# Performance work log

Measured on AMD Instinct MI355X. Metric: run time of the kernel, lower is better.

The kernel has to match this reference:

```python
import jax, jax.numpy as jnp
import numpy as np

D_MODEL = 1024
N_HEADS = 16
D_HEAD = D_MODEL // N_HEADS
MAX_K_LEN = 1024
SYNTH_HIDDEN = 1024
B, TQ, TK = 2, 1024, 1024
CAUSAL = True


def setup_inputs() -> dict:
    key = jax.random.key(0)
    ks = jax.random.split(key, 12)
    s = 1.0 / np.sqrt(D_MODEL)
    inp = {
        "x_q": jax.random.normal(ks[0], (B, TQ, D_MODEL), jnp.float32),
        "x_kv": jax.random.normal(ks[1], (B, TK, D_MODEL), jnp.float32),
        "key_padding_mask": jnp.ones((B, TK), jnp.int32),
        # projection weights stored [in, out] (equivalent to torch Linear)
        "Wq": jax.random.normal(ks[2], (D_MODEL, D_MODEL), jnp.float32) * s,
        "bq": jnp.zeros((D_MODEL,), jnp.float32),
        "Wk": jax.random.normal(ks[3], (D_MODEL, D_MODEL), jnp.float32) * s,
        "bk": jnp.zeros((D_MODEL,), jnp.float32),
        "Wv": jax.random.normal(ks[4], (D_MODEL, D_MODEL), jnp.float32) * s,
        "bv": jnp.zeros((D_MODEL,), jnp.float32),
        "Wo": jax.random.normal(ks[5], (D_MODEL, D_MODEL), jnp.float32) * s,
        "bo": jnp.zeros((D_MODEL,), jnp.float32),
        # synthesizer MLP: d_model -> synth_hidden -> n_heads*max_k_len
        "Ws1": jax.random.normal(ks[6], (D_MODEL, SYNTH_HIDDEN), jnp.float32) * s,
        "bs1": jnp.zeros((SYNTH_HIDDEN,), jnp.float32),
        "Ws2": jax.random.normal(ks[7], (SYNTH_HIDDEN, N_HEADS * MAX_K_LEN), jnp.float32) * (1.0 / np.sqrt(SYNTH_HIDDEN)),
        "bs2": jnp.zeros((N_HEADS * MAX_K_LEN,), jnp.float32),
        # gate logits init at log(0.5/0.5) = 0 -> sigmoid = 0.5
        "gate": jnp.zeros((N_HEADS,), jnp.float32),
    }
    return inp


def _attention(x_q, x_kv, key_padding_mask, Wq, bq, Wk, bk, Wv, bv, Wo, bo,
               Ws1, bs1, Ws2, bs2, gate):
    B_, Tq, _ = x_q.shape
    Tk = x_kv.shape[1]
    scale = D_HEAD ** -0.5

    def shape_heads(x):  # [B,T,D] -> [B,H,T,dh]
        return x.reshape(B_, -1, N_HEADS, D_HEAD).transpose(0, 2, 1, 3)

    Q = shape_heads(x_q @ Wq + bq)
    K = shape_heads(x_kv @ Wk + bk)
    V = shape_heads(x_kv @ Wv + bv)

    vanilla = jnp.einsum("bhqd,bhkd->bhqk", Q, K) * scale

    # dense synthesizer: MLP(x_q) -> [B,Tq,H,max_k_len] -> [B,H,Tq,Tk]
    h = jax.nn.gelu(x_q @ Ws1 + bs1, approximate=False)
    S = (h @ Ws2 + bs2).reshape(B_, Tq, N_HEADS, MAX_K_LEN)
    synth = S.transpose(0, 2, 1, 3)[:, :, :, :Tk]

    g = jax.nn.sigmoid(gate).reshape(1, N_HEADS, 1, 1)
    logits = (1.0 - g) * vanilla + g * synth

    # key padding mask: 1 = keep, 0 = pad
    keep = (key_padding_mask > 0).reshape(B_, 1, 1, Tk)
    logits = jnp.where(keep, logits, -jnp.inf)
    if CAUSAL:
        causal_mask = jnp.tril(jnp.ones((Tq, Tk), bool))  # keep lower triangle
        logits = jnp.where(causal_mask, logits, -jnp.inf)

    attn = jax.nn.softmax(logits, axis=-1)
    ctx = jnp.einsum("bhqk,bhkd->bhqd", attn, V)
    out = ctx.transpose(0, 2, 1, 3).reshape(B_, Tq, D_MODEL)
    return out @ Wo + bo


def reference(x_q, x_kv, key_padding_mask, Wq, bq, Wk, bk, Wv, bv, Wo, bo,
              Ws1, bs1, Ws2, bs2, gate):
    return _attention(x_q, x_kv, key_padding_mask, Wq, bq, Wk, bk, Wv, bv,
                      Wo, bo, Ws1, bs1, Ws2, bs2, gate)
```

## Files before the change

kernel.cpp:

```cpp
#include <hip/hip_runtime.h>
#include <hip/hip_bf16.h>

#define D_MODEL 1024
#define N_HEADS 16
#define MAX_K_LEN 1024
#define B_SZ 2
#define TQ 1024
#define TK 1024
#define M_ROWS 2048
#define NKL 16384

using bf16x8 = __attribute__((ext_vector_type(8))) short;
using f32x4  = __attribute__((ext_vector_type(4))) float;
using u16x8  = __attribute__((ext_vector_type(8))) unsigned short;

__device__ __forceinline__ unsigned short f2b(float f) {
    unsigned u = __float_as_uint(f);
    u = (u + 0x7FFFu + ((u >> 16) & 1u)) >> 16;
    return (unsigned short)u;
}
__device__ __forceinline__ float b2f(unsigned short u) {
    return __uint_as_float(((unsigned)u) << 16);
}

__device__ __forceinline__ void async_cp16(void* lds, const void* g) {
    __builtin_amdgcn_global_load_lds(
        (__attribute__((address_space(1))) void*)(void*)g,
        (__attribute__((address_space(3))) void*)lds, 16, 0, 0);
}

__device__ __forceinline__ int xrow(int row) {
    return (row & 7) ^ (((row >> 3) & 3) << 1);
}

__device__ __forceinline__ void ptile128_core(
    const unsigned short* __restrict__ A, const unsigned short* __restrict__ Wt,
    const float* __restrict__ bias, unsigned short* __restrict__ C,
    int N, int m0g, int n0g, int act, const float* __restrict__ gate,
    unsigned short* lds)
{
    constexpr int NT = 32;
    const int tid = threadIdx.x;
    const int lane = tid & 63;
    const int fr = lane & 15, rg = lane >> 4;
    const int w = tid >> 6;
    const int wr = w >> 1, wc = w & 1;

    const int sr = tid >> 2;
    const int sc = ((tid & 3) ^ ((sr >> 1) & 3)) * 8;
    const unsigned short* gA = A  + (size_t)(m0g + sr) * 1024 + sc;
    const unsigned short* gB = Wt + (size_t)(n0g + sr) * 1024 + sc;

    auto stage = [&](int t) {
        unsigned short* bufA = lds + (t % 3) * 8192;
        unsigned short* bufB = bufA + 4096;
        const int k0 = t * 32;
        async_cp16(bufA + tid*8,        gA + k0);
        async_cp16(bufA + 2048 + tid*8, gA + (size_t)64*1024 + k0);
        async_cp16(bufB + tid*8,        gB + k0);
        async_cp16(bufB + 2048 + tid*8, gB + (size_t)64*1024 + k0);
    };

    f32x4 acc[4][4];
#pragma unroll
    for (int i = 0; i < 4; ++i)
#pragma unroll
        for (int j = 0; j < 4; ++j) { f32x4 z = {0.f,0.f,0.f,0.f}; acc[i][j] = z; }

    const int fko = (rg ^ ((fr >> 1) & 3)) * 8;

    stage(0); stage(1);
    asm volatile("s_waitcnt vmcnt(4)" ::: "memory");
    __builtin_amdgcn_s_barrier();
    __builtin_amdgcn_sched_barrier(0);

    for (int t = 0; t < NT; ++t) {
        const unsigned short* bufA = lds + (t % 3) * 8192;
        const unsigned short* bufB = bufA + 4096;

        bf16x8 afr[4], bfr[4];
#pragma unroll
        for (int mi = 0; mi < 4; ++mi)
            afr[mi] = *(const bf16x8*)(bufA + (wr*64 + mi*16 + fr)*32 + fko);
#pragma unroll
        for (int ni = 0; ni < 4; ++ni)
            bfr[ni] = *(const bf16x8*)(bufB + (wc*64 + ni*16 + fr)*32 + fko);
        if (t + 2 < NT) stage(t + 2);

        __builtin_amdgcn_s_setprio(1);
#pragma unroll
        for (int mi = 0; mi < 4; ++mi)
#pragma unroll
            for (int ni = 0; ni < 4; ++ni)
                acc[mi][ni] = __builtin_amdgcn_mfma_f32_16x16x32_bf16(
                    afr[mi], bfr[ni], acc[mi][ni], 0, 0, 0);
        __builtin_amdgcn_s_setprio(0);

        if (t < NT - 2)       asm volatile("s_waitcnt vmcnt(4)" ::: "memory");
        else if (t == NT - 2) asm volatile("s_waitcnt vmcnt(0)" ::: "memory");
        __builtin_amdgcn_s_barrier();
        __builtin_amdgcn_sched_barrier(0);
    }

    float qs = 1.f;
    if (act == 2) {
        const float gg = 1.f / (1.f + __expf(-gate[(n0g + wc*64) >> 6]));
        qs = (1.f - gg) * 0.125f;
    }

    unsigned short* scr = lds + w * 1024;
    float bv[4];
#pragma unroll
    for (int ni = 0; ni < 4; ++ni) bv[ni] = bias[n0g + wc*64 + ni*16 + fr];
    const int ro = lane >> 3;
    const int co = (lane & 7) * 8;
#pragma unroll
    for (int mi = 0; mi < 4; ++mi) {
#pragma unroll
        for (int ni = 0; ni < 4; ++ni)
#pragma unroll
            for (int r = 0; r < 4; ++r) {
                float c = acc[mi][ni][r] + bv[ni];
                if (act == 1) c = 0.5f * c * (1.f + erff(c * 0.70710678118654752f));
                else if (act == 2) c *= qs;
                scr[(rg*4 + r)*64 + ni*16 + fr] = f2b(c);
            }
#pragma unroll
        for (int p = 0; p < 2; ++p) {
            const int row = p*8 + ro;
            const u16x8 v = *(const u16x8*)(scr + row*64 + co);
            *(u16x8*)(C + (size_t)(m0g + wr*64 + mi*16 + row) * N + n0g + wc*64 + co) = v;
        }
    }
}

struct QkvhArgs {
    const unsigned short* A[4];
    const unsigned short* W[4];
    const float* bias[4];
    void* out[4];
    const float* gate;
};

__global__ __launch_bounds__(256, 3) void gemm_qkvh_p(QkvhArgs args) {
    __shared__ __align__(16) unsigned short lds[24576];
    const int z = blockIdx.z;
    const int m0 = (blockIdx.x >> 3) * 128;
    const int n0 = (blockIdx.x & 7) * 128;
    const int act = (z == 3) ? 1 : ((z == 0) ? 2 : 0);
    ptile128_core(args.A[z], args.W[z], args.bias[z],
                  (unsigned short*)args.out[z], D_MODEL, m0, n0, act, args.gate, lds);
}

__global__ __launch_bounds__(256, 3) void gemm_logits_p(
    const unsigned short* __restrict__ A, const unsigned short* __restrict__ Wt,
    const float* __restrict__ bias, unsigned short* __restrict__ C,
    const unsigned short* __restrict__ Qpre, const unsigned short* __restrict__ Kb)
{
    __shared__ __align__(16) unsigned short lds[24576];
    constexpr int NT = 34;
    const int bid = blockIdx.x;
    const int xcd = bid & 7;
    const int i = bid >> 3;
    const int hi = (i >= 72) ? 1 : 0;
    const int head = xcd * 2 + hi;
    const int j = i - hi * 72;
    int kq, idx;
    if (j < 16)      { kq = 0; idx = j; }
    else if (j < 30) { kq = 1; idx = j - 16; }
    else if (j < 42) { kq = 2; idx = j - 30; }
    else if (j < 52) { kq = 3; idx = j - 42; }
    else if (j < 60) { kq = 4; idx = j - 52; }
    else if (j < 66) { kq = 5; idx = j - 60; }
    else if (j < 70) { kq = 6; idx = j - 66; }
    else             { kq = 7; idx = j - 70; }
    const int b = idx & 1;
    const int rq = kq + (idx >> 1);
    const int m0g = (b * 8 + rq) * 128;
    const int n0g = (head * 8 + kq) * 128;

    const int tid = threadIdx.x;
    const int lane = tid & 63;
    const int fr = lane & 15, rg = lane >> 4;
    const int w = tid >> 6;
    const int wr = w >> 1, wc = w & 1;

    const int sr = tid >> 2;
    const int sc = ((tid & 3) ^ ((sr >> 1) & 3)) * 8;
    const unsigned short* gA = A  + (size_t)(m0g + sr) * 1024 + sc;
    const unsigned short* gB = Wt + (size_t)(n0g + sr) * 1024 + sc;
    const int q0 = rq * 128, k0a = kq * 128;
    const unsigned short* gA2 = Qpre + (size_t)(b*TQ + q0 + sr) * 1024 + head*64 + sc;
    const unsigned short* gB2 = Kb   + (size_t)(b*TK + k0a + sr) * 1024 + head*64 + sc;

    auto stageQK = [&](int t) {
        unsigned short* bufA = lds + (t % 3) * 8192;
        unsigned short* bufB = bufA + 4096;
        const int k0 = t * 32;
        async_cp16(bufA + tid*8,        gA2 + k0);
        async_cp16(bufA + 2048 + tid*8, gA2 + (size_t)64*1024 + k0);
        async_cp16(bufB + tid*8,        gB2 + k0);
        async_cp16(bufB + 2048 + tid*8, gB2 + (size_t)64*1024 + k0);
    };
    auto stageS = [&](int t) {
        unsigned short* bufA = lds + (t % 3) * 8192;
        unsigned short* bufB = bufA + 4096;
        const int k0 = (t - 2) * 32;
        async_cp16(bufA + tid*8,        gA + k0);
        async_cp16(bufA + 2048 + tid*8, gA + (size_t)64*1024 + k0);
        async_cp16(bufB + tid*8,        gB + k0);
        async_cp16(bufB + 2048 + tid*8, gB + (size_t)64*1024 + k0);
    };

    f32x4 acc[4][4];
#pragma unroll
    for (int ii = 0; ii < 4; ++ii)
#pragma unroll
        for (int jj = 0; jj < 4; ++jj) { f32x4 z = {0.f,0.f,0.f,0.f}; acc[ii][jj] = z; }

    const int fko = (rg ^ ((fr >> 1) & 3)) * 8;

    stageQK(0); stageQK(1);
    asm volatile("s_waitcnt vmcnt(4)" ::: "memory");
    __builtin_amdgcn_s_barrier();
    __builtin_amdgcn_sched_barrier(0);

    for (int t = 0; t < NT; ++t) {
        const unsigned short* bufA = lds + (t % 3) * 8192;
        const unsigned short* bufB = bufA + 4096;

        bf16x8 afr[4], bfr[4];
#pragma unroll
        for (int mi = 0; mi < 4; ++mi)
            afr[mi] = *(const bf16x8*)(bufA + (wr*64 + mi*16 + fr)*32 + fko);
#pragma unroll
        for (int ni = 0; ni < 4; ++ni)
            bfr[ni] = *(const bf16x8*)(bufB + (wc*64 + ni*16 + fr)*32 + fko);
        if (t + 2 < NT) stageS(t + 2);

        __builtin_amdgcn_s_setprio(1);
#pragma unroll
        for (int mi = 0; mi < 4; ++mi)
#pragma unroll
            for (int ni = 0; ni < 4; ++ni)
                acc[mi][ni] = __builtin_amdgcn_mfma_f32_16x16x32_bf16(
                    afr[mi], bfr[ni], acc[mi][ni], 0, 0, 0);
        __builtin_amdgcn_s_setprio(0);

        if (t < NT - 2)       asm volatile("s_waitcnt vmcnt(4)" ::: "memory");
        else if (t == NT - 2) asm volatile("s_waitcnt vmcnt(0)" ::: "memory");
        __builtin_amdgcn_s_barrier();
        __builtin_amdgcn_sched_barrier(0);
    }

    unsigned short* scr = lds + w * 1024;
    float bv[4];
#pragma unroll
    for (int ni = 0; ni < 4; ++ni) bv[ni] = bias[n0g + wc*64 + ni*16 + fr];
    const int ro = lane >> 3;
    const int co = (lane & 7) * 8;
#pragma unroll
    for (int mi = 0; mi < 4; ++mi) {
#pragma unroll
        for (int ni = 0; ni < 4; ++ni)
#pragma unroll
            for (int r = 0; r < 4; ++r)
                scr[(rg*4 + r)*64 + ni*16 + fr] = f2b(acc[mi][ni][r] + bv[ni]);
#pragma unroll
        for (int p = 0; p < 2; ++p) {
            const int row = p*8 + ro;
            const u16x8 v = *(const u16x8*)(scr + row*64 + co);
            *(u16x8*)(C + (size_t)(m0g + wr*64 + mi*16 + row) * NKL + n0g + wc*64 + co) = v;
        }
    }
}

__global__ __launch_bounds__(256, 3) void gemm_out_p(
    const unsigned short* __restrict__ A, const unsigned short* __restrict__ Wt,
    const float* __restrict__ bias, float* __restrict__ C)
{
    __shared__ __align__(16) unsigned short lds[24576];
    constexpr int NT = 32;
    const int m0g = blockIdx.y * 128;
    const int n0g = blockIdx.x * 128;

    const int tid = threadIdx.x;
    const int lane = tid & 63;
    const int fr = lane & 15, rg = lane >> 4;
    const int w = tid >> 6;
    const int wr = w >> 1, wc = w & 1;

    const int sr = tid >> 2;
    const int sc = ((tid & 3) ^ ((sr >> 1) & 3)) * 8;
    const unsigned short* gA = A  + (size_t)(m0g + sr) * 1024 + sc;
    const unsigned short* gB = Wt + (size_t)(n0g + sr) * 1024 + sc;

    auto stage = [&](int t) {
        unsigned short* bufA = lds + (t % 3) * 8192;
        unsigned short* bufB = bufA + 4096;
        const int k0 = t * 32;
        async_cp16(bufA + tid*8,        gA + k0);
        async_cp16(bufA + 2048 + tid*8, gA + (size_t)64*1024 + k0);
        async_cp16(bufB + tid*8,        gB + k0);
        async_cp16(bufB + 2048 + tid*8, gB + (size_t)64*1024 + k0);
    };

    f32x4 acc[4][4];
#pragma unroll
    for (int i = 0; i < 4; ++i)
#pragma unroll
        for (int j = 0; j < 4; ++j) { f32x4 z = {0.f,0.f,0.f,0.f}; acc[i][j] = z; }

    const int fko = (rg ^ ((fr >> 1) & 3)) * 8;

    stage(0); stage(1);
    asm volatile("s_waitcnt vmcnt(4)" ::: "memory");
    __builtin_amdgcn_s_barrier();
    __builtin_amdgcn_sched_barrier(0);

    for (int t = 0; t < NT; ++t) {
        const unsigned short* bufA = lds + (t % 3) * 8192;
        const unsigned short* bufB = bufA + 4096;

        bf16x8 afr[4], bfr[4];
#pragma unroll
        for (int mi = 0; mi < 4; ++mi)
            afr[mi] = *(const bf16x8*)(bufA + (wr*64 + mi*16 + fr)*32 + fko);
#pragma unroll
        for (int ni = 0; ni < 4; ++ni)
            bfr[ni] = *(const bf16x8*)(bufB + (wc*64 + ni*16 + fr)*32 + fko);
        if (t + 2 < NT) stage(t + 2);

        __builtin_amdgcn_s_setprio(1);
#pragma unroll
        for (int mi = 0; mi < 4; ++mi)
#pragma unroll
            for (int ni = 0; ni < 4; ++ni)
                acc[mi][ni] = __builtin_amdgcn_mfma_f32_16x16x32_bf16(
                    afr[mi], bfr[ni], acc[mi][ni], 0, 0, 0);
        __builtin_amdgcn_s_setprio(0);

        if (t < NT - 2)       asm volatile("s_waitcnt vmcnt(4)" ::: "memory");
        else if (t == NT - 2) asm volatile("s_waitcnt vmcnt(0)" ::: "memory");
        __builtin_amdgcn_s_barrier();
        __builtin_amdgcn_sched_barrier(0);
    }

#pragma unroll
    for (int ni = 0; ni < 4; ++ni) {
        const int colx = n0g + wc*64 + ni*16 + fr;
        const float bvv = bias[colx];
#pragma unroll
        for (int mi = 0; mi < 4; ++mi)
#pragma unroll
            for (int r = 0; r < 4; ++r) {
                const int row = m0g + wr*64 + mi*16 + rg*4 + r;
                C[(size_t)row * D_MODEL + colx] = acc[mi][ni][r] + bvv;
            }
    }
}

struct PrepArgs {
    const float* xq; const float* xkv;
    unsigned short* xq_b; unsigned short* xkv_b;
    const float* W[6]; unsigned short* Wt[6]; int Nw[6];
    const float* bs2; float* bs2g; const float* gate;
};

__global__ __launch_bounds__(256) void prep_all(PrepArgs p) {
    __shared__ float T[32][33];
    int id = blockIdx.x;
    if (id < 4096) {
        const float* src = (id < 2048) ? p.xq : p.xkv;
        unsigned short* dst = (id < 2048) ? p.xq_b : p.xkv_b;
        const int i = (id & 2047) * 256 + threadIdx.x;
        const float4 v = ((const float4*)src)[i];
        ushort4 o; o.x = f2b(v.x); o.y = f2b(v.y); o.z = f2b(v.z); o.w = f2b(v.w);
        ((ushort4*)dst)[i] = o;
        return;
    }
    if (id >= 25600) {
        const int i = (id - 25600) * 256 + threadIdx.x;
        const float gg = 1.f / (1.f + __expf(-p.gate[i >> 10]));
        p.bs2g[i] = gg * p.bs2[i];
        return;
    }
    id -= 4096;
    int seg, lb;
    if (id < 5120) { seg = id >> 10; lb = id & 1023; }
    else           { seg = 5;        lb = id - 5120; }
    const int N = p.Nw[seg];
    const int nx = N >> 5;
    const int bx = lb % nx, by = lb / nx;
    const int n0 = bx * 32, k0 = by * 32;
    const float* W = p.W[seg];
    unsigned short* Wt = p.Wt[seg];
    float gs = 1.f;
    if (seg == 5) gs = 1.f / (1.f + __expf(-p.gate[n0 >> 10]));
    const int r = threadIdx.x >> 3, c = (threadIdx.x & 7) * 4;
    const float4 v = *(const float4*)&W[(size_t)(k0 + r) * N + n0 + c];
    T[r][c] = v.x; T[r][c+1] = v.y; T[r][c+2] = v.z; T[r][c+3] = v.w;
    __syncthreads();
    ushort4 o;
    o.x = f2b(T[c][r] * gs); o.y = f2b(T[c+1][r] * gs);
    o.z = f2b(T[c+2][r] * gs); o.w = f2b(T[c+3][r] * gs);
    *(ushort4*)&Wt[(size_t)(n0 + r) * D_MODEL + k0 + c] = o;
}

__global__ __launch_bounds__(256) void attn_l(
    const unsigned short* __restrict__ Lb, const unsigned short* __restrict__ Vb,
    const int* __restrict__ kpm, unsigned short* __restrict__ ctx)
{
    const int bx = blockIdx.x;
    const int q1 = bx >> 1;
    const int qt = (bx & 1) ? q1 : (15 - q1);
    const int h = blockIdx.y, b = blockIdx.z;
    const int tid = threadIdx.x;
    const int lane = tid & 63;
    const int w = tid >> 6;
    const int col = lane & 15, rg = lane >> 4;
    const int q0g = qt * 64;

    __shared__ __align__(16) unsigned short Ls[2][64*64];
    __shared__ __align__(16) unsigned short Vt[2][64*64];
    __shared__ __align__(16) unsigned short Pl[4*16*64];

    const int srr = tid >> 3, scp = tid & 7;
    auto issueL = [&](int kt, int buf) {
        const unsigned short* gs = Lb + ((size_t)(b*TQ + q0g)) * NKL + h*MAX_K_LEN + kt*64;
        async_cp16(Ls[buf] + tid*8,        gs + (size_t)srr*NKL + (scp ^ xrow(srr))*8);
        async_cp16(Ls[buf] + 2048 + tid*8, gs + (size_t)(srr+32)*NKL + (scp ^ xrow(srr+32))*8);
    };
    const int vk = tid >> 2, vdc = (tid & 3) * 16;
    const int vkc = vk >> 3, vke = vk & 7;
    u16x8 vr0, vr1;
    auto loadV = [&](int kt) {
        const unsigned short* gv = Vb + ((size_t)(b*TK + kt*64 + vk)) * D_MODEL + h*64 + vdc;
        vr0 = *(const u16x8*)gv;
        vr1 = *(const u16x8*)(gv + 8);
    };
    auto writeV = [&](int buf) {
#pragma unroll
        for (int j = 0; j < 8; ++j) {
            const int d0 = vdc + j, d1 = vdc + 8 + j;
            Vt[buf][d0*64 + (vkc ^ xrow(d0))*8 + vke] = vr0[j];
            Vt[buf][d1*64 + (vkc ^ xrow(d1))*8 + vke] = vr1[j];
        }
    };

    issueL(0, 0);
    loadV(0);
    writeV(0);
    __syncthreads();

    unsigned short* Pw = Pl + w*(16*64);

    float mrun[4] = {-INFINITY,-INFINITY,-INFINITY,-INFINITY};
    float lrun[4] = {0.f,0.f,0.f,0.f};
    f32x4 octx[4];
#pragma unroll
    for (int n = 0; n < 4; ++n) { f32x4 z = {0.f,0.f,0.f,0.f}; octx[n] = z; }

    for (int kt = 0; kt <= qt; ++kt) {
        const int cur = kt & 1;

        int kvalid[4];
#pragma unroll
        for (int n = 0; n < 4; ++n)
            kvalid[n] = kpm[b*TK + kt*64 + n*16 + col];
        if (kt < qt) { issueL(kt + 1, cur ^ 1); loadV(kt + 1); }

        const bool diag = (kt == qt);
        float acc[4][4];
        float tmax[4] = {-INFINITY,-INFINITY,-INFINITY,-INFINITY};
#pragma unroll
        for (int n = 0; n < 4; ++n) {
            const int kl = n*16 + col;
#pragma unroll
            for (int r = 0; r < 4; ++r) {
                const int ql = w*16 + rg*4 + r;
                const float lv = b2f(Ls[cur][ql*64 + (((kl>>3) ^ xrow(ql)))*8 + (kl&7)]);
                const bool ok = (kvalid[n] > 0) && (!diag || kl <= ql);
                const float sv = ok ? lv : -INFINITY;
                acc[n][r] = sv;
                tmax[r] = fmaxf(tmax[r], sv);
            }
        }
#pragma unroll
        for (int o = 1; o < 16; o <<= 1) {
#pragma unroll
            for (int r = 0; r < 4; ++r) tmax[r] = fmaxf(tmax[r], __shfl_xor(tmax[r], o));
        }
        float sc[4];
#pragma unroll
        for (int r = 0; r < 4; ++r) {
            const float mn = fmaxf(mrun[r], tmax[r]);
            sc[r] = (mrun[r] == -INFINITY) ? 0.f : __expf(mrun[r] - mn);
            mrun[r] = mn;
        }
        float tsum[4] = {0.f,0.f,0.f,0.f};
#pragma unroll
        for (int n = 0; n < 4; ++n)
#pragma unroll
            for (int r = 0; r < 4; ++r) {
                const float pz = (acc[n][r] == -INFINITY) ? 0.f : __expf(acc[n][r] - mrun[r]);
                acc[n][r] = pz;
                tsum[r] += pz;
            }
#pragma unroll
        for (int o = 1; o < 16; o <<= 1) {
#pragma unroll
            for (int r = 0; r < 4; ++r) tsum[r] += __shfl_xor(tsum[r], o);
        }
#pragma unroll
        for (int r = 0; r < 4; ++r) lrun[r] = lrun[r]*sc[r] + tsum[r];
#pragma unroll
        for (int n = 0; n < 4; ++n)
#pragma unroll
            for (int r = 0; r < 4; ++r) octx[n][r] *= sc[r];

#pragma unroll
        for (int n = 0; n < 4; ++n) {
            const int kc = n*16 + col;
#pragma unroll
            for (int r = 0; r < 4; ++r) {
                const int q = rg*4 + r;
                Pw[q*64 + (((kc>>3) ^ xrow(q)))*8 + (kc&7)] = f2b(acc[n][r]);
            }
        }

#pragma unroll
        for (int ks = 0; ks < 2; ++ks) {
            const bf16x8 pa = *(const bf16x8*)(Pw + col*64 + ((ks*4 + rg) ^ xrow(col))*8);
#pragma unroll
            for (int n = 0; n < 4; ++n) {
                const int d = n*16 + col;
                const bf16x8 vv = *(const bf16x8*)(Vt[cur] + d*64 + ((ks*4 + rg) ^ xrow(d))*8);
                octx[n] = __builtin_amdgcn_mfma_f32_16x16x32_bf16(pa, vv, octx[n], 0, 0, 0);
            }
        }

        if (kt < qt) writeV(cur ^ 1);
        __syncthreads();
    }

    float inv[4];
#pragma unroll
    for (int r = 0; r < 4; ++r) inv[r] = (lrun[r] > 0.f) ? 1.f/lrun[r] : 0.f;
#pragma unroll
    for (int n = 0; n < 4; ++n)
#pragma unroll
        for (int r = 0; r < 4; ++r) {
            const size_t row = (size_t)(b*TQ + q0g + w*16 + rg*4 + r);
            ctx[row*D_MODEL + h*64 + n*16 + col] = f2b(octx[n][r]*inv[r]);
        }
}

extern "C" void kernel_launch(void* const* d_in, const int* in_sizes, int n_in,
                              void* d_out, int out_size, void* d_ws, size_t ws_size,
                              hipStream_t stream) {
    const float* x_q  = (const float*)d_in[0];
    const float* x_kv = (const float*)d_in[1];
    const int*   kpm  = (const int*)d_in[2];
    const float* Wq  = (const float*)d_in[3];  const float* bq  = (const float*)d_in[4];
    const float* Wk  = (const float*)d_in[5];  const float* bk  = (const float*)d_in[6];
    const float* Wv  = (const float*)d_in[7];  const float* bv  = (const float*)d_in[8];
    const float* Wo  = (const float*)d_in[9];  const float* bo  = (const float*)d_in[10];
    const float* Ws1 = (const float*)d_in[11]; const float* bs1 = (const float*)d_in[12];
    const float* Ws2 = (const float*)d_in[13]; const float* bs2 = (const float*)d_in[14];
    const float* gate = (const float*)d_in[15];

    char* ws = (char*)d_ws;
    const size_t MB = 1024ull * 1024ull;
    unsigned short* Sb    = (unsigned short*)ws;
    unsigned short* xq_b  = (unsigned short*)ws;
    unsigned short* xkv_b = (unsigned short*)(ws + 4*MB);
    size_t off = 64*MB;
    unsigned short* Wq_t  = (unsigned short*)(ws + off); off += 2*MB;
    unsigned short* Wk_t  = (unsigned short*)(ws + off); off += 2*MB;
    unsigned short* Wv_t  = (unsigned short*)(ws + off); off += 2*MB;
    unsigned short* Wo_t  = (unsigned short*)(ws + off); off += 2*MB;
    unsigned short* Ws1_t = (unsigned short*)(ws + off); off += 2*MB;
    unsigned short* Ws2_t = (unsigned short*)(ws + off); off += 32*MB;
    unsigned short* Qb    = (unsigned short*)(ws + off); off += 4*MB;
    unsigned short* Kb    = (unsigned short*)(ws + off); off += 4*MB;
    unsigned short* Vb    = (unsigned short*)(ws + off); off += 4*MB;
    unsigned short* hb    = (unsigned short*)(ws + off); off += 4*MB;
    unsigned short* ctxb  = (unsigned short*)(ws + off); off += 4*MB;
    float* bs2g           = (float*)(ws + off); off += 64*1024;

    dim3 blk(256);

    PrepArgs pa;
    pa.xq = x_q; pa.xkv = x_kv; pa.xq_b = xq_b; pa.xkv_b = xkv_b;
    pa.W[0] = Wq;  pa.Wt[0] = Wq_t;  pa.Nw[0] = D_MODEL;
    pa.W[1] = Wk;  pa.Wt[1] = Wk_t;  pa.Nw[1] = D_MODEL;
    pa.W[2] = Wv;  pa.Wt[2] = Wv_t;  pa.Nw[2] = D_MODEL;
    pa.W[3] = Wo;  pa.Wt[3] = Wo_t;  pa.Nw[3] = D_MODEL;
    pa.W[4] = Ws1; pa.Wt[4] = Ws1_t; pa.Nw[4] = D_MODEL;
    pa.W[5] = Ws2; pa.Wt[5] = Ws2_t; pa.Nw[5] = NKL;
    pa.bs2 = bs2; pa.bs2g = bs2g; pa.gate = gate;
    prep_all<<<dim3(25664), blk, 0, stream>>>(pa);

    QkvhArgs qa;
    qa.A[0] = xq_b;  qa.W[0] = Wq_t;  qa.bias[0] = bq;  qa.out[0] = Qb;
    qa.A[1] = xkv_b; qa.W[1] = Wk_t;  qa.bias[1] = bk;  qa.out[1] = Kb;
    qa.A[2] = xkv_b; qa.W[2] = Wv_t;  qa.bias[2] = bv;  qa.out[2] = Vb;
    qa.A[3] = xq_b;  qa.W[3] = Ws1_t; qa.bias[3] = bs1; qa.out[3] = hb;
    qa.gate = gate;
    gemm_qkvh_p<<<dim3(128, 1, 4), dim3(256), 0, stream>>>(qa);

    gemm_logits_p<<<dim3(1152), dim3(256), 0, stream>>>(hb, Ws2_t, bs2g, Sb, Qb, Kb);

    attn_l<<<dim3(TQ/64, N_HEADS, B_SZ), blk, 0, stream>>>(Sb, Vb, kpm, ctxb);

    gemm_out_p<<<dim3(8, 16), dim3(256), 0, stream>>>(ctxb, Wo_t, bo, (float*)d_out);
}
```

Baseline: 165.7 us.

## Split softmax into a row-statistics pass and a P·V pass with masks applied in the GEMM epilogue

The causal and padding masks move into the logits GEMM epilogue, which writes -inf bf16 for masked entries. A new rowstat kernel computes each row's max and inverse sum. The attention kernel then becomes a plain exp-normalize-and-MFMA over V, with no online-softmax rescaling, cross-lane reductions or LDS round trip for P. The cost is an extra kernel launch and a second read of the logits tensor, about 32MB of bf16 in the causal half.

Measured after the change: 170.4 us. 1.03x slower.

```diff
diff --git a/kernel.cpp b/kernel.cpp
--- a/kernel.cpp
+++ b/kernel.cpp
@@ -155,7 +155,8 @@
 __global__ __launch_bounds__(256, 3) void gemm_logits_p(
     const unsigned short* __restrict__ A, const unsigned short* __restrict__ Wt,
     const float* __restrict__ bias, unsigned short* __restrict__ C,
-    const unsigned short* __restrict__ Qpre, const unsigned short* __restrict__ Kb)
+    const unsigned short* __restrict__ Qpre, const unsigned short* __restrict__ Kb,
+    const int* __restrict__ kpm)
 {
     __shared__ __align__(16) unsigned short lds[24576];
     constexpr int NT = 34;
@@ -255,17 +256,28 @@
 
     unsigned short* scr = lds + w * 1024;
     float bv[4];
-#pragma unroll
-    for (int ni = 0; ni < 4; ++ni) bv[ni] = bias[n0g + wc*64 + ni*16 + fr];
+    int kv[4];
+#pragma unroll
+    for (int ni = 0; ni < 4; ++ni) {
+        const int colx = n0g + wc*64 + ni*16 + fr;
+        bv[ni] = bias[colx];
+        kv[ni] = kpm[b * TK + (colx & 1023)];
+    }
     const int ro = lane >> 3;
     const int co = (lane & 7) * 8;
 #pragma unroll
     for (int mi = 0; mi < 4; ++mi) {
 #pragma unroll
-        for (int ni = 0; ni < 4; ++ni)
-#pragma unroll
-            for (int r = 0; r < 4; ++r)
-                scr[(rg*4 + r)*64 + ni*16 + fr] = f2b(acc[mi][ni][r] + bv[ni]);
+        for (int ni = 0; ni < 4; ++ni) {
+            const int k_idx = (n0g + wc*64 + ni*16 + fr) & 1023;
+#pragma unroll
+            for (int r = 0; r < 4; ++r) {
+                const int q_idx = (m0g + wr*64 + mi*16 + rg*4 + r) & 1023;
+                const bool ok = (kv[ni] > 0) && (k_idx <= q_idx);
+                scr[(rg*4 + r)*64 + ni*16 + fr] =
+                    ok ? f2b(acc[mi][ni][r] + bv[ni]) : (unsigned short)0xFF80u;
+            }
+        }
 #pragma unroll
         for (int p = 0; p < 2; ++p) {
             const int row = p*8 + ro;
@@ -407,9 +419,47 @@
     *(ushort4*)&Wt[(size_t)(n0 + r) * D_MODEL + k0 + c] = o;
 }
 
-__global__ __launch_bounds__(256) void attn_l(
+__global__ __launch_bounds__(256) void rowstat(
+    const unsigned short* __restrict__ Lb,
+    float* __restrict__ Ms, float* __restrict__ Is)
+{
+    const int id = blockIdx.x * 4 + (threadIdx.x >> 6);
+    const int lane = threadIdx.x & 63;
+    const int row = id >> 4;
+    const int h = id & 15;
+    const int q = row & 1023;
+    const unsigned short* src = Lb + (size_t)row * NKL + h * MAX_K_LEN + lane;
+    const int nj = (q >> 6) + 1;
+
+    float vals[16];
+    float vmax = -INFINITY;
+#pragma unroll
+    for (int j = 0; j < 16; ++j) {
+        if (j < nj) {
+            vals[j] = b2f(src[j * 64]);
+            vmax = fmaxf(vmax, vals[j]);
+        } else vals[j] = -INFINITY;
+    }
+#pragma unroll
+    for (int o = 32; o; o >>= 1) vmax = fmaxf(vmax, __shfl_xor(vmax, o));
+
+    float s = 0.f;
+#pragma unroll
+    for (int j = 0; j < 16; ++j)
+        if (j < nj && vals[j] != -INFINITY) s += __expf(vals[j] - vmax);
+#pragma unroll
+    for (int o = 32; o; o >>= 1) s += __shfl_xor(s, o);
+
+    if (lane == 0) {
+        if (vmax == -INFINITY) { Ms[row * 16 + h] = 0.f; Is[row * 16 + h] = 0.f; }
+        else { Ms[row * 16 + h] = vmax; Is[row * 16 + h] = 1.f / s; }
+    }
+}
+
+__global__ __launch_bounds__(256) void attn_pv(
     const unsigned short* __restrict__ Lb, const unsigned short* __restrict__ Vb,
-    const int* __restrict__ kpm, unsigned short* __restrict__ ctx)
+    const float* __restrict__ Ms, const float* __restrict__ Is,
+    unsigned short* __restrict__ ctx)
 {
     const int bx = blockIdx.x;
     const int q1 = bx >> 1;
@@ -423,7 +473,6 @@
 
     __shared__ __align__(16) unsigned short Ls[2][64*64];
     __shared__ __align__(16) unsigned short Vt[2][64*64];
-    __shared__ __align__(16) unsigned short Pl[4*16*64];
 
     const int srr = tid >> 3, scp = tid & 7;
     auto issueL = [&](int kt, int buf) {
@@ -448,94 +497,37 @@
         }
     };
 
+    const int qrow = q0g + w*16 + col;
+    const float m_row  = Ms[((size_t)(b*1024 + qrow)) * 16 + h];
+    const float inv_row = Is[((size_t)(b*1024 + qrow)) * 16 + h];
+
     issueL(0, 0);
     loadV(0);
     writeV(0);
     __syncthreads();
 
-    unsigned short* Pw = Pl + w*(16*64);
-
-    float mrun[4] = {-INFINITY,-INFINITY,-INFINITY,-INFINITY};
-    float lrun[4] = {0.f,0.f,0.f,0.f};
     f32x4 octx[4];
 #pragma unroll
     for (int n = 0; n < 4; ++n) { f32x4 z = {0.f,0.f,0.f,0.f}; octx[n] = z; }
 
     for (int kt = 0; kt <= qt; ++kt) {
         const int cur = kt & 1;
-
-        int kvalid[4];
-#pragma unroll
-        for (int n = 0; n < 4; ++n)
-            kvalid[n] = kpm[b*TK + kt*64 + n*16 + col];
         if (kt < qt) { issueL(kt + 1, cur ^ 1); loadV(kt + 1); }
 
-        const bool diag = (kt == qt);
-        float acc[4][4];
-        float tmax[4] = {-INFINITY,-INFINITY,-INFINITY,-INFINITY};
-#pragma unroll
-        for (int n = 0; n < 4; ++n) {
-            const int kl = n*16 + col;
-#pragma unroll
-            for (int r = 0; r < 4; ++r) {
-                const int ql = w*16 + rg*4 + r;
-                const float lv = b2f(Ls[cur][ql*64 + (((kl>>3) ^ xrow(ql)))*8 + (kl&7)]);
-                const bool ok = (kvalid[n] > 0) && (!diag || kl <= ql);
-                const float sv = ok ? lv : -INFINITY;
-                acc[n][r] = sv;
-                tmax[r] = fmaxf(tmax[r], sv);
+#pragma unroll
+        for (int s = 0; s < 2; ++s) {
+            const int lrow = w*16 + col;
+            const bf16x8 lf = *(const bf16x8*)(Ls[cur] + lrow*64 + ((s*4 + rg) ^ xrow(lrow))*8);
+            bf16x8 pa;
+#pragma unroll
+            for (int jj = 0; jj < 8; ++jj) {
+                const float p = __expf(b2f((unsigned short)lf[jj]) - m_row) * inv_row;
+                pa[jj] = (short)f2b(p);
             }
-        }
-#pragma unroll
-        for (int o = 1; o < 16; o <<= 1) {
-#pragma unroll
-            for (int r = 0; r < 4; ++r) tmax[r] = fmaxf(tmax[r], __shfl_xor(tmax[r], o));
-        }
-        float sc[4];
-#pragma unroll
-        for (int r = 0; r < 4; ++r) {
-            const float mn = fmaxf(mrun[r], tmax[r]);
-            sc[r] = (mrun[r] == -INFINITY) ? 0.f : __expf(mrun[r] - mn);
-            mrun[r] = mn;
-        }
-        float tsum[4] = {0.f,0.f,0.f,0.f};
-#pragma unroll
-        for (int n = 0; n < 4; ++n)
-#pragma unroll
-            for (int r = 0; r < 4; ++r) {
-                const float pz = (acc[n][r] == -INFINITY) ? 0.f : __expf(acc[n][r] - mrun[r]);
-                acc[n][r] = pz;
-                tsum[r] += pz;
-            }
-#pragma unroll
-        for (int o = 1; o < 16; o <<= 1) {
-#pragma unroll
-            for (int r = 0; r < 4; ++r) tsum[r] += __shfl_xor(tsum[r], o);
-        }
-#pragma unroll
-        for (int r = 0; r < 4; ++r) lrun[r] = lrun[r]*sc[r] + tsum[r];
-#pragma unroll
-        for (int n = 0; n < 4; ++n)
-#pragma unroll
-            for (int r = 0; r < 4; ++r) octx[n][r] *= sc[r];
-
-#pragma unroll
-        for (int n = 0; n < 4; ++n) {
-            const int kc = n*16 + col;
-#pragma unroll
-            for (int r = 0; r < 4; ++r) {
-                const int q = rg*4 + r;
-                Pw[q*64 + (((kc>>3) ^ xrow(q)))*8 + (kc&7)] = f2b(acc[n][r]);
-            }
-        }
-
-#pragma unroll
-        for (int ks = 0; ks < 2; ++ks) {
-            const bf16x8 pa = *(const bf16x8*)(Pw + col*64 + ((ks*4 + rg) ^ xrow(col))*8);
 #pragma unroll
             for (int n = 0; n < 4; ++n) {
                 const int d = n*16 + col;
-                const bf16x8 vv = *(const bf16x8*)(Vt[cur] + d*64 + ((ks*4 + rg) ^ xrow(d))*8);
+                const bf16x8 vv = *(const bf16x8*)(Vt[cur] + d*64 + ((s*4 + rg) ^ xrow(d))*8);
                 octx[n] = __builtin_amdgcn_mfma_f32_16x16x32_bf16(pa, vv, octx[n], 0, 0, 0);
             }
         }
@@ -544,15 +536,12 @@
         __syncthreads();
     }
 
-    float inv[4];
-#pragma unroll
-    for (int r = 0; r < 4; ++r) inv[r] = (lrun[r] > 0.f) ? 1.f/lrun[r] : 0.f;
 #pragma unroll
     for (int n = 0; n < 4; ++n)
 #pragma unroll
         for (int r = 0; r < 4; ++r) {
             const size_t row = (size_t)(b*TQ + q0g + w*16 + rg*4 + r);
-            ctx[row*D_MODEL + h*64 + n*16 + col] = f2b(octx[n][r]*inv[r]);
+            ctx[row*D_MODEL + h*64 + n*16 + col] = f2b(octx[n][r]);
         }
 }
 
@@ -588,6 +577,8 @@
     unsigned short* hb    = (unsigned short*)(ws + off); off += 4*MB;
     unsigned short* ctxb  = (unsigned short*)(ws + off); off += 4*MB;
     float* bs2g           = (float*)(ws + off); off += 64*1024;
+    float* Ms             = (float*)(ws + off); off += 128*1024;
+    float* Is             = (float*)(ws + off); off += 128*1024;
 
     dim3 blk(256);
 
@@ -610,9 +601,11 @@
     qa.gate = gate;
     gemm_qkvh_p<<<dim3(128, 1, 4), dim3(256), 0, stream>>>(qa);
 
-    gemm_logits_p<<<dim3(1152), dim3(256), 0, stream>>>(hb, Ws2_t, bs2g, Sb, Qb, Kb);
-
-    attn_l<<<dim3(TQ/64, N_HEADS, B_SZ), blk, 0, stream>>>(Sb, Vb, kpm, ctxb);
+    gemm_logits_p<<<dim3(1152), dim3(256), 0, stream>>>(hb, Ws2_t, bs2g, Sb, Qb, Kb, kpm);
+
+    rowstat<<<dim3(8192), blk, 0, stream>>>(Sb, Ms, Is);
+
+    attn_pv<<<dim3(TQ/64, N_HEADS, B_SZ), blk, 0, stream>>>(Sb, Vb, Ms, Is, ctxb);
 
     gemm_out_p<<<dim3(8, 16), dim3(256), 0, stream>>>(ctxb, Wo_t, bo, (float*)d_out);
 }
```
